# Kernel optimization log

Measured on AMD Instinct MI355X. Metric: run time of the kernel, lower is better.

Reference implementation:

```python
import jax, jax.numpy as jnp
import numpy as np

NUM_HEADS = 8
HEAD_SIZE = 64  # hidden_dim // num_heads = 512 // 8
SCALE = 1.0 / np.sqrt(HEAD_SIZE).astype(np.float32)
CAUSAL = True


def setup_inputs() -> dict:
    key = jax.random.key(0)
    k1, k2, k3 = jax.random.split(key, 3)
    b, s, d = 4, 2048, 512
    x = jax.random.normal(k1, (b, s, d), dtype=jnp.float32)
    w_qkv = jax.random.normal(k2, (d, 3 * d), dtype=jnp.float32) * 0.02
    b_qkv = jnp.zeros((3 * d,), dtype=jnp.float32)
    w_out = jax.random.normal(k3, (d, d), dtype=jnp.float32) * 0.02
    b_out = jnp.zeros((d,), dtype=jnp.float32)
    return {"x": x, "w_qkv": w_qkv, "b_qkv": b_qkv, "w_out": w_out, "b_out": b_out}


def reference(x, w_qkv, b_qkv, w_out, b_out):
    b, s, d = x.shape
    h, hd = NUM_HEADS, HEAD_SIZE
    qkv = x @ w_qkv + b_qkv                      # (b, s, 3d)
    q, k, v = jnp.split(qkv, 3, axis=-1)
    # (b, s, d) -> (b, h, s, hd)
    q = q.reshape(b, s, h, hd).transpose(0, 2, 1, 3)
    k = k.reshape(b, s, h, hd).transpose(0, 2, 1, 3)
    v = v.reshape(b, s, h, hd).transpose(0, 2, 1, 3)
    scores = jnp.einsum('bhqd,bhkd->bhqk', q, k) * SCALE  # (b, h, s, s)
    if CAUSAL:
        causal_mask = jnp.triu(jnp.ones((s, s), dtype=bool), k=1)
        scores = jnp.where(causal_mask, -jnp.inf, scores)
    attn = jax.nn.softmax(scores, axis=-1)
    out = jnp.einsum('bhqk,bhkd->bhqd', attn, v)          # (b, h, s, hd)
    out = out.transpose(0, 2, 1, 3).reshape(b, s, d)
    return out @ w_out + b_out
```

## Files before the change

kernel.cpp:

```cpp
#include <hip/hip_runtime.h>

#define BATCH 4
#define SEQ   2048
#define DM    512
#define NH    8
#define HD    64
#define PART  (BATCH*NH*SEQ*HD)
#define QSCALE 0.18033688f

typedef unsigned short u16;
typedef unsigned int   u32;
typedef __bf16 bf16x8 __attribute__((ext_vector_type(8)));
typedef float  f32x4  __attribute__((ext_vector_type(4)));

__device__ __forceinline__ u16 f2bf(float f) {
    union { float f; u32 u; } v; v.f = f;
    u32 r = v.u + 0x7fffu + ((v.u >> 16) & 1u);
    return (u16)(r >> 16);
}

__device__ __forceinline__ void glds16(const u16* g, u16* lds) {
    __builtin_amdgcn_global_load_lds(
        (const __attribute__((address_space(1))) void*)g,
        (__attribute__((address_space(3))) void*)lds, 16, 0, 0);
}

__global__ __launch_bounds__(256) void cvt_k(
    const float* __restrict__ src, u16* __restrict__ dst, int n8)
{
    for (int i = blockIdx.x * 256 + threadIdx.x; i < n8;
         i += gridDim.x * 256) {
        float4 a = *(const float4*)(src + (size_t)i * 8);
        float4 b = *(const float4*)(src + (size_t)i * 8 + 4);
        union { uint4 v; u16 s[8]; } o;
        o.s[0] = f2bf(a.x); o.s[1] = f2bf(a.y);
        o.s[2] = f2bf(a.z); o.s[3] = f2bf(a.w);
        o.s[4] = f2bf(b.x); o.s[5] = f2bf(b.y);
        o.s[6] = f2bf(b.z); o.s[7] = f2bf(b.w);
        *(uint4*)(dst + (size_t)i * 8) = o.v;
    }
}

__global__ __launch_bounds__(256) void transpose_k(
    const float* __restrict__ W0, u16* __restrict__ T0,
    const float* __restrict__ W1, u16* __restrict__ T1)
{
    const int z = blockIdx.z;
    const int N = z ? DM : 3 * DM;
    if ((int)blockIdx.x * 64 >= N) return;
    const float* W = z ? W1 : W0;
    u16* Wt = z ? T1 : T0;

    __shared__ u16 Ts[64][72];
    const int t = threadIdx.x;
    const int n0 = blockIdx.x * 64, k0 = blockIdx.y * 64;
    #pragma unroll
    for (int l = 0; l < 4; ++l) {
        int idx = l * 1024 + t * 4;
        int r = idx >> 6, c = idx & 63;
        float4 v = *(const float4*)(W + (size_t)(k0 + r) * N + n0 + c);
        Ts[c + 0][r] = f2bf(v.x);
        Ts[c + 1][r] = f2bf(v.y);
        Ts[c + 2][r] = f2bf(v.z);
        Ts[c + 3][r] = f2bf(v.w);
    }
    __syncthreads();
    #pragma unroll
    for (int l = 0; l < 2; ++l) {
        int idx = l * 256 + t;
        int row = idx >> 3, ch = idx & 7;
        *(uint4*)(Wt + (size_t)(n0 + row) * DM + k0 + ch * 8) =
            *(const uint4*)(&Ts[row][ch * 8]);
    }
}

template<int MODE>
__global__ __launch_bounds__(256) void gemm_k(
    const u16* __restrict__ A, const u16* __restrict__ Bt,
    const float* __restrict__ bias, void* __restrict__ outv,
    int M, int N, int K)
{
    __shared__ __align__(16) u16 As[128 * 32];
    __shared__ __align__(16) u16 Bs[128 * 32];

    const int tid  = threadIdx.x;
    const int bm0  = blockIdx.x * 128;
    const int bn0  = blockIdx.y * 128;
    const int wave = tid >> 6, lane = tid & 63;
    const int l16  = lane & 15, quad = lane >> 4;
    const int wr   = (wave & 1) * 64;
    const int wc   = (wave >> 1) * 64;

    const int srow = (lane >> 2);
    const int scol = (lane & 3) * 8;
    const u16* Ag = A + (size_t)(bm0 + wave * 32 + srow) * K + scol;
    const u16* Bg = Bt + (size_t)(bn0 + wave * 32 + srow) * K + scol;
    u16* AsB = &As[(wave * 32) * 32];
    u16* BsB = &Bs[(wave * 32) * 32];

    f32x4 acc[4][4];
    #pragma unroll
    for (int i = 0; i < 4; ++i)
        #pragma unroll
        for (int j = 0; j < 4; ++j)
            acc[i][j] = (f32x4){0.f, 0.f, 0.f, 0.f};

    for (int k0 = 0; k0 < K; k0 += 32) {
        glds16(Ag + k0,                  AsB);
        glds16(Ag + k0 + (size_t)16 * K, AsB + 16 * 32);
        glds16(Bg + k0,                  BsB);
        glds16(Bg + k0 + (size_t)16 * K, BsB + 16 * 32);
        __syncthreads();

        bf16x8 af[4], bfr[4];
        #pragma unroll
        for (int mi = 0; mi < 4; ++mi)
            af[mi] = *(const bf16x8*)(&As[(wr + mi * 16 + l16) * 32 + quad * 8]);
        #pragma unroll
        for (int ni = 0; ni < 4; ++ni)
            bfr[ni] = *(const bf16x8*)(&Bs[(wc + ni * 16 + l16) * 32 + quad * 8]);
        #pragma unroll
        for (int mi = 0; mi < 4; ++mi)
            #pragma unroll
            for (int ni = 0; ni < 4; ++ni)
                acc[mi][ni] = __builtin_amdgcn_mfma_f32_16x16x32_bf16(
                    af[mi], bfr[ni], acc[mi][ni], 0, 0, 0);
        __syncthreads();
    }

    #pragma unroll
    for (int mi = 0; mi < 4; ++mi) {
        #pragma unroll
        for (int ni = 0; ni < 4; ++ni) {
            int col = bn0 + wc + ni * 16 + l16;
            float bv = bias[col];
            int row0 = bm0 + wr + mi * 16 + quad * 4;
            float v[4];
            #pragma unroll
            for (int reg = 0; reg < 4; ++reg) v[reg] = acc[mi][ni][reg] + bv;

            if (MODE == 1) {
                #pragma unroll
                for (int reg = 0; reg < 4; ++reg)
                    ((float*)outv)[(size_t)(row0 + reg) * N + col] = v[reg];
            } else {
                u16* ws = (u16*)outv;
                int part = col >> 9, wi = col & 511;
                int h = wi >> 6, e = wi & 63;
                int b = row0 >> 11, s0 = row0 & 2047;
                if (part == 2) {
                    union { u16 q[4]; uint2 u; } pk;
                    #pragma unroll
                    for (int reg = 0; reg < 4; ++reg) pk.q[reg] = f2bf(v[reg]);
                    *(uint2*)(ws + (size_t)2 * PART +
                              ((size_t)(b * NH + h) * HD + e) * SEQ + s0) = pk.u;
                } else {
                    float scl = (part == 0) ? QSCALE : 1.0f;
                    #pragma unroll
                    for (int reg = 0; reg < 4; ++reg)
                        ws[(size_t)part * PART +
                           ((size_t)(b * NH + h) * SEQ + s0 + reg) * HD + e] =
                            f2bf(v[reg] * scl);
                }
            }
        }
    }
}

__global__ __launch_bounds__(256) void attn_k(
    const u16* __restrict__ Q, const u16* __restrict__ K,
    const u16* __restrict__ Vt, u16* __restrict__ O)
{
    __shared__ __align__(16) u16 KsB[2][64 * 64];
    __shared__ __align__(16) u16 VtB[2][64 * 64];
    __shared__ __align__(16) u16 Ps[128][72];

    const int bh = blockIdx.y;
    const int qb = (blockIdx.y & 16) ? (int)blockIdx.x : (15 - (int)blockIdx.x);
    const int tid = threadIdx.x, wave = tid >> 6, lane = tid & 63;
    const int l16 = lane & 15, quad = lane >> 4;
    const size_t baseK = (size_t)bh * SEQ * HD;
    const size_t baseV = (size_t)bh * HD * SEQ;
    const size_t baseQ = baseK + (size_t)qb * 128 * HD;

    #pragma unroll
    for (int r = 0; r < 4; ++r) {
        int chunk = r * 256 + tid;
        int row = chunk >> 3, c8 = (chunk & 7) << 3;
        *(uint4*)(&Ps[row][c8]) = *(const uint4*)(Q + baseQ + row * 64 + c8);
    }
    __syncthreads();

    bf16x8 qf[2][2];
    #pragma unroll
    for (int rf = 0; rf < 2; ++rf)
        #pragma unroll
        for (int d0 = 0; d0 < 2; ++d0)
            qf[rf][d0] = *(const bf16x8*)(&Ps[rf * 64 + wave * 16 + l16]
                                            [d0 * 32 + quad * 8]);

    const int sub = lane >> 3;
    const int lcx = (lane & 7) ^ sub;
    const u16* kg = K  + baseK + (size_t)((wave * 16 + sub) * 64)  + lcx * 8;
    const u16* vg = Vt + baseV + (size_t)((wave * 16 + sub) * 2048) + lcx * 8;
    u16* ksd = &KsB[0][wave * 1024];
    u16* vtd = &VtB[0][wave * 1024];

    glds16(kg,                 ksd);
    glds16(kg + 8 * 64,        ksd + 512);
    glds16(vg,                 vtd);
    glds16(vg + 8 * 2048,      vtd + 512);
    __syncthreads();

    float l_part[2][4];
    f32x4 o_acc[2][4];
    #pragma unroll
    for (int rf = 0; rf < 2; ++rf)
        #pragma unroll
        for (int i = 0; i < 4; ++i) {
            l_part[rf][i] = 0.f;
            o_acc[rf][i] = (f32x4){0.f, 0.f, 0.f, 0.f};
        }

    const int last = 2 * qb + 1;
    const int row64 = wave * 16 + quad * 4;

    for (int kt = 0; kt <= last; ++kt) {
        const int cur = kt & 1;

        if (kt < last) {
            const int nx = (cur ^ 1) * 4096;
            glds16(kg + (size_t)(kt + 1) * 4096,            ksd + nx);
            glds16(kg + (size_t)(kt + 1) * 4096 + 8 * 64,   ksd + nx + 512);
            glds16(vg + (size_t)(kt + 1) * 64,              vtd + nx);
            glds16(vg + (size_t)(kt + 1) * 64 + 8 * 2048,   vtd + nx + 512);
        }

        bf16x8 kf[2][4];
        #pragma unroll
        for (int d0 = 0; d0 < 2; ++d0)
            #pragma unroll
            for (int nt = 0; nt < 4; ++nt) {
                int pc = (d0 * 4 + quad) ^ (l16 & 7);
                kf[d0][nt] = *(const bf16x8*)
                    (&KsB[cur][(nt * 16 + l16) * 64 + pc * 8]);
            }

        #pragma unroll
        for (int rf = 0; rf < 2; ++rf) {
            if (kt == last && rf == 0) continue;
            f32x4 s[4];
            #pragma unroll
            for (int nt = 0; nt < 4; ++nt) s[nt] = (f32x4){0.f, 0.f, 0.f, 0.f};
            #pragma unroll
            for (int d0 = 0; d0 < 2; ++d0)
                #pragma unroll
                for (int nt = 0; nt < 4; ++nt)
                    s[nt] = __builtin_amdgcn_mfma_f32_16x16x32_bf16(
                        qf[rf][d0], kf[d0][nt], s[nt], 0, 0, 0);

            const bool diag = (kt == 2 * qb + rf);
            if (diag) {
                #pragma unroll
                for (int nt = 0; nt < 4; ++nt) {
                    int cl = nt * 16 + l16;
                    #pragma unroll
                    for (int reg = 0; reg < 4; ++reg) {
                        float p = (cl > row64 + reg) ? 0.f
                                : __builtin_amdgcn_exp2f(s[nt][reg]);
                        l_part[rf][reg] += p;
                        Ps[rf * 64 + row64 + reg][cl] = f2bf(p);
                    }
                }
            } else {
                #pragma unroll
                for (int nt = 0; nt < 4; ++nt) {
                    int cl = nt * 16 + l16;
                    #pragma unroll
                    for (int reg = 0; reg < 4; ++reg) {
                        float p = __builtin_amdgcn_exp2f(s[nt][reg]);
                        l_part[rf][reg] += p;
                        Ps[rf * 64 + row64 + reg][cl] = f2bf(p);
                    }
                }
            }
        }
        __syncthreads();

        bf16x8 vf[2][4];
        #pragma unroll
        for (int k0 = 0; k0 < 2; ++k0)
            #pragma unroll
            for (int dt = 0; dt < 4; ++dt) {
                int pc = (k0 * 4 + quad) ^ (l16 & 7);
                vf[k0][dt] = *(const bf16x8*)
                    (&VtB[cur][(dt * 16 + l16) * 64 + pc * 8]);
            }
        #pragma unroll
        for (int rf = 0; rf < 2; ++rf) {
            if (kt == last && rf == 0) continue;
            #pragma unroll
            for (int k0 = 0; k0 < 2; ++k0) {
                bf16x8 ap = *(const bf16x8*)
                    (&Ps[rf * 64 + wave * 16 + l16][k0 * 32 + quad * 8]);
                #pragma unroll
                for (int dt = 0; dt < 4; ++dt)
                    o_acc[rf][dt] = __builtin_amdgcn_mfma_f32_16x16x32_bf16(
                        ap, vf[k0][dt], o_acc[rf][dt], 0, 0, 0);
            }
        }
        __syncthreads();
    }

    const int b = bh >> 3, h = bh & 7;
    #pragma unroll
    for (int rf = 0; rf < 2; ++rf) {
        float l_i[4];
        #pragma unroll
        for (int reg = 0; reg < 4; ++reg) {
            float l = l_part[rf][reg];
            #pragma unroll
            for (int off = 1; off < 16; off <<= 1)
                l += __shfl_xor(l, off);
            l_i[reg] = l;
        }
        #pragma unroll
        for (int dt = 0; dt < 4; ++dt) {
            #pragma unroll
            for (int reg = 0; reg < 4; ++reg) {
                int srow = qb * 128 + rf * 64 + row64 + reg;
                float v = o_acc[rf][dt][reg] / l_i[reg];
                size_t idx = (((size_t)(b * SEQ + srow)) * NH + h) * HD
                             + dt * 16 + l16;
                O[idx] = f2bf(v);
            }
        }
    }
}

extern "C" void kernel_launch(void* const* d_in, const int* in_sizes, int n_in,
                              void* d_out, int out_size, void* d_ws, size_t ws_size,
                              hipStream_t stream) {
    const float* x     = (const float*)d_in[0];
    const float* w_qkv = (const float*)d_in[1];
    const float* b_qkv = (const float*)d_in[2];
    const float* w_out = (const float*)d_in[3];
    const float* b_out = (const float*)d_in[4];

    u16* qkv    = (u16*)d_ws;
    u16* attn   = qkv + (size_t)3 * PART;
    u16* xb     = attn + (size_t)PART;
    u16* wt_qkv = xb + (size_t)PART;
    u16* wt_out = wt_qkv + (size_t)(3 * DM) * DM;

    const int M = BATCH * SEQ;

    cvt_k<<<1024, 256, 0, stream>>>(x, xb, PART / 8);
    transpose_k<<<dim3(24, 8, 2), 256, 0, stream>>>(w_qkv, wt_qkv, w_out, wt_out);

    dim3 g1(M / 128, (3 * DM) / 128);
    gemm_k<0><<<g1, 256, 0, stream>>>(xb, wt_qkv, b_qkv, qkv, M, 3 * DM, DM);

    dim3 g2(16, BATCH * NH);
    attn_k<<<g2, 256, 0, stream>>>(qkv, qkv + PART, qkv + 2 * (size_t)PART, attn);

    dim3 g3(M / 128, DM / 128);
    gemm_k<1><<<g3, 256, 0, stream>>>(attn, wt_out, b_out, (float*)d_out, M, DM, DM);
}
```

Before: 172.2 us.

## Merge prep kernels, double-buffer GEMM LDS, drop attention sync, swap grid axes

Folds the fp32-to-bf16 conversion of x and the two weight transposes into one prep kernel launched on a 3-slice grid. The GEMM now double-buffers its A/B LDS tiles, so the next K-slice loads while MFMAs run on the current one. The attention kernel loads V fragments together with K fragments and does the P·V MFMAs right after writing P, dropping the mid-iteration barrier. This works because each wave only reads back the P rows it wrote itself. It also swaps grid axes so batch-head varies fastest, and replaces the diagonal branch with a predicated mask. The costs are extra LDS in the GEMM and more live registers in attention.

```diff
diff --git a/kernel.cpp b/kernel.cpp
--- a/kernel.cpp
+++ b/kernel.cpp
@@ -25,35 +25,35 @@
         (__attribute__((address_space(3))) void*)lds, 16, 0, 0);
 }
 
-__global__ __launch_bounds__(256) void cvt_k(
-    const float* __restrict__ src, u16* __restrict__ dst, int n8)
+__global__ __launch_bounds__(256) void prep_k(
+    const float* __restrict__ x, u16* __restrict__ xb,
+    const float* __restrict__ w_qkv, u16* __restrict__ t_qkv,
+    const float* __restrict__ w_out, u16* __restrict__ t_out)
 {
-    for (int i = blockIdx.x * 256 + threadIdx.x; i < n8;
-         i += gridDim.x * 256) {
-        float4 a = *(const float4*)(src + (size_t)i * 8);
-        float4 b = *(const float4*)(src + (size_t)i * 8 + 4);
-        union { uint4 v; u16 s[8]; } o;
-        o.s[0] = f2bf(a.x); o.s[1] = f2bf(a.y);
-        o.s[2] = f2bf(a.z); o.s[3] = f2bf(a.w);
-        o.s[4] = f2bf(b.x); o.s[5] = f2bf(b.y);
-        o.s[6] = f2bf(b.z); o.s[7] = f2bf(b.w);
-        *(uint4*)(dst + (size_t)i * 8) = o.v;
-    }
-}
-
-__global__ __launch_bounds__(256) void transpose_k(
-    const float* __restrict__ W0, u16* __restrict__ T0,
-    const float* __restrict__ W1, u16* __restrict__ T1)
-{
-    const int z = blockIdx.z;
-    const int N = z ? DM : 3 * DM;
-    if ((int)blockIdx.x * 64 >= N) return;
-    const float* W = z ? W1 : W0;
-    u16* Wt = z ? T1 : T0;
-
     __shared__ u16 Ts[64][72];
-    const int t = threadIdx.x;
-    const int n0 = blockIdx.x * 64, k0 = blockIdx.y * 64;
+    const int z = blockIdx.z, bx = blockIdx.x, t = threadIdx.x;
+
+    if (z == 0) {
+        const int n8 = PART / 8;
+        for (int i = bx * 256 + t; i < n8; i += 512 * 256) {
+            float4 a = *(const float4*)(x + (size_t)i * 8);
+            float4 b = *(const float4*)(x + (size_t)i * 8 + 4);
+            union { uint4 v; u16 s[8]; } o;
+            o.s[0] = f2bf(a.x); o.s[1] = f2bf(a.y);
+            o.s[2] = f2bf(a.z); o.s[3] = f2bf(a.w);
+            o.s[4] = f2bf(b.x); o.s[5] = f2bf(b.y);
+            o.s[6] = f2bf(b.z); o.s[7] = f2bf(b.w);
+            *(uint4*)(xb + (size_t)i * 8) = o.v;
+        }
+        return;
+    }
+    const int N = (z == 1) ? 3 * DM : DM;
+    const int ntiles = N / 64;
+    if (bx >= ntiles * 8) return;
+    const float* W = (z == 1) ? w_qkv : w_out;
+    u16* Wt = (z == 1) ? t_qkv : t_out;
+    const int n0 = (bx % ntiles) * 64, k0 = (bx / ntiles) * 64;
+
     #pragma unroll
     for (int l = 0; l < 4; ++l) {
         int idx = l * 1024 + t * 4;
@@ -80,8 +80,8 @@
     const float* __restrict__ bias, void* __restrict__ outv,
     int M, int N, int K)
 {
-    __shared__ __align__(16) u16 As[128 * 32];
-    __shared__ __align__(16) u16 Bs[128 * 32];
+    __shared__ __align__(16) u16 As[2][128 * 32];
+    __shared__ __align__(16) u16 Bs[2][128 * 32];
 
     const int tid  = threadIdx.x;
     const int bm0  = blockIdx.x * 128;
@@ -95,8 +95,7 @@
     const int scol = (lane & 3) * 8;
     const u16* Ag = A + (size_t)(bm0 + wave * 32 + srow) * K + scol;
     const u16* Bg = Bt + (size_t)(bn0 + wave * 32 + srow) * K + scol;
-    u16* AsB = &As[(wave * 32) * 32];
-    u16* BsB = &Bs[(wave * 32) * 32];
+    const int wofs = (wave * 32) * 32;
 
     f32x4 acc[4][4];
     #pragma unroll
@@ -105,20 +104,31 @@
         for (int j = 0; j < 4; ++j)
             acc[i][j] = (f32x4){0.f, 0.f, 0.f, 0.f};
 
-    for (int k0 = 0; k0 < K; k0 += 32) {
-        glds16(Ag + k0,                  AsB);
-        glds16(Ag + k0 + (size_t)16 * K, AsB + 16 * 32);
-        glds16(Bg + k0,                  BsB);
-        glds16(Bg + k0 + (size_t)16 * K, BsB + 16 * 32);
-        __syncthreads();
+    glds16(Ag,                  &As[0][wofs]);
+    glds16(Ag + (size_t)16 * K, &As[0][wofs + 16 * 32]);
+    glds16(Bg,                  &Bs[0][wofs]);
+    glds16(Bg + (size_t)16 * K, &Bs[0][wofs + 16 * 32]);
+    __syncthreads();
+
+    const int NIT = K >> 5;
+    for (int it = 0; it < NIT; ++it) {
+        const int cur = it & 1;
+        if (it + 1 < NIT) {
+            const int nx = cur ^ 1;
+            const int k0 = (it + 1) << 5;
+            glds16(Ag + k0,                  &As[nx][wofs]);
+            glds16(Ag + k0 + (size_t)16 * K, &As[nx][wofs + 16 * 32]);
+            glds16(Bg + k0,                  &Bs[nx][wofs]);
+            glds16(Bg + k0 + (size_t)16 * K, &Bs[nx][wofs + 16 * 32]);
+        }
 
         bf16x8 af[4], bfr[4];
         #pragma unroll
         for (int mi = 0; mi < 4; ++mi)
-            af[mi] = *(const bf16x8*)(&As[(wr + mi * 16 + l16) * 32 + quad * 8]);
+            af[mi] = *(const bf16x8*)(&As[cur][(wr + mi * 16 + l16) * 32 + quad * 8]);
         #pragma unroll
         for (int ni = 0; ni < 4; ++ni)
-            bfr[ni] = *(const bf16x8*)(&Bs[(wc + ni * 16 + l16) * 32 + quad * 8]);
+            bfr[ni] = *(const bf16x8*)(&Bs[cur][(wc + ni * 16 + l16) * 32 + quad * 8]);
         #pragma unroll
         for (int mi = 0; mi < 4; ++mi)
             #pragma unroll
@@ -175,8 +185,9 @@
     __shared__ __align__(16) u16 VtB[2][64 * 64];
     __shared__ __align__(16) u16 Ps[128][72];
 
-    const int bh = blockIdx.y;
-    const int qb = (blockIdx.y & 16) ? (int)blockIdx.x : (15 - (int)blockIdx.x);
+    const int bh = blockIdx.x;
+    const int yy = blockIdx.y;
+    const int qb = (yy < 8) ? (15 - yy) : (yy - 8);
     const int tid = threadIdx.x, wave = tid >> 6, lane = tid & 63;
     const int l16 = lane & 15, quad = lane >> 4;
     const size_t baseK = (size_t)bh * SEQ * HD;
@@ -201,15 +212,15 @@
 
     const int sub = lane >> 3;
     const int lcx = (lane & 7) ^ sub;
-    const u16* kg = K  + baseK + (size_t)((wave * 16 + sub) * 64)  + lcx * 8;
+    const u16* kg = K  + baseK + (size_t)((wave * 16 + sub) * 64)   + lcx * 8;
     const u16* vg = Vt + baseV + (size_t)((wave * 16 + sub) * 2048) + lcx * 8;
     u16* ksd = &KsB[0][wave * 1024];
     u16* vtd = &VtB[0][wave * 1024];
 
-    glds16(kg,                 ksd);
-    glds16(kg + 8 * 64,        ksd + 512);
-    glds16(vg,                 vtd);
-    glds16(vg + 8 * 2048,      vtd + 512);
+    glds16(kg,            ksd);
+    glds16(kg + 8 * 64,   ksd + 512);
+    glds16(vg,            vtd);
+    glds16(vg + 8 * 2048, vtd + 512);
     __syncthreads();
 
     float l_part[2][4];
@@ -230,13 +241,13 @@
 
         if (kt < last) {
             const int nx = (cur ^ 1) * 4096;
-            glds16(kg + (size_t)(kt + 1) * 4096,            ksd + nx);
-            glds16(kg + (size_t)(kt + 1) * 4096 + 8 * 64,   ksd + nx + 512);
-            glds16(vg + (size_t)(kt + 1) * 64,              vtd + nx);
-            glds16(vg + (size_t)(kt + 1) * 64 + 8 * 2048,   vtd + nx + 512);
-        }
-
-        bf16x8 kf[2][4];
+            glds16(kg + (size_t)(kt + 1) * 4096,          ksd + nx);
+            glds16(kg + (size_t)(kt + 1) * 4096 + 8 * 64, ksd + nx + 512);
+            glds16(vg + (size_t)(kt + 1) * 64,            vtd + nx);
+            glds16(vg + (size_t)(kt + 1) * 64 + 8 * 2048, vtd + nx + 512);
+        }
+
+        bf16x8 kf[2][4], vf[2][4];
         #pragma unroll
         for (int d0 = 0; d0 < 2; ++d0)
             #pragma unroll
@@ -244,6 +255,8 @@
                 int pc = (d0 * 4 + quad) ^ (l16 & 7);
                 kf[d0][nt] = *(const bf16x8*)
                     (&KsB[cur][(nt * 16 + l16) * 64 + pc * 8]);
+                vf[d0][nt] = *(const bf16x8*)
+                    (&VtB[cur][(nt * 16 + l16) * 64 + pc * 8]);
             }
 
         #pragma unroll
@@ -260,45 +273,18 @@
                         qf[rf][d0], kf[d0][nt], s[nt], 0, 0, 0);
 
             const bool diag = (kt == 2 * qb + rf);
-            if (diag) {
+            #pragma unroll
+            for (int nt = 0; nt < 4; ++nt) {
+                int cl = nt * 16 + l16;
                 #pragma unroll
-                for (int nt = 0; nt < 4; ++nt) {
-                    int cl = nt * 16 + l16;
-                    #pragma unroll
-                    for (int reg = 0; reg < 4; ++reg) {
-                        float p = (cl > row64 + reg) ? 0.f
-                                : __builtin_amdgcn_exp2f(s[nt][reg]);
-                        l_part[rf][reg] += p;
-                        Ps[rf * 64 + row64 + reg][cl] = f2bf(p);
-                    }
+                for (int reg = 0; reg < 4; ++reg) {
+                    float p = __builtin_amdgcn_exp2f(s[nt][reg]);
+                    if (diag && cl > row64 + reg) p = 0.f;
+                    l_part[rf][reg] += p;
+                    Ps[rf * 64 + row64 + reg][cl] = f2bf(p);
                 }
-            } else {
-                #pragma unroll
-                for (int nt = 0; nt < 4; ++nt) {
-                    int cl = nt * 16 + l16;
-                    #pragma unroll
-                    for (int reg = 0; reg < 4; ++reg) {
-                        float p = __builtin_amdgcn_exp2f(s[nt][reg]);
-                        l_part[rf][reg] += p;
-                        Ps[rf * 64 + row64 + reg][cl] = f2bf(p);
-                    }
-                }
-            }
-        }
-        __syncthreads();
-
-        bf16x8 vf[2][4];
-        #pragma unroll
-        for (int k0 = 0; k0 < 2; ++k0)
-            #pragma unroll
-            for (int dt = 0; dt < 4; ++dt) {
-                int pc = (k0 * 4 + quad) ^ (l16 & 7);
-                vf[k0][dt] = *(const bf16x8*)
-                    (&VtB[cur][(dt * 16 + l16) * 64 + pc * 8]);
-            }
-        #pragma unroll
-        for (int rf = 0; rf < 2; ++rf) {
-            if (kt == last && rf == 0) continue;
+            }
+
             #pragma unroll
             for (int k0 = 0; k0 < 2; ++k0) {
                 bf16x8 ap = *(const bf16x8*)
@@ -355,13 +341,13 @@
 
     const int M = BATCH * SEQ;
 
-    cvt_k<<<1024, 256, 0, stream>>>(x, xb, PART / 8);
-    transpose_k<<<dim3(24, 8, 2), 256, 0, stream>>>(w_qkv, wt_qkv, w_out, wt_out);
+    prep_k<<<dim3(512, 1, 3), 256, 0, stream>>>(x, xb, w_qkv, wt_qkv,
+                                                w_out, wt_out);
 
     dim3 g1(M / 128, (3 * DM) / 128);
     gemm_k<0><<<g1, 256, 0, stream>>>(xb, wt_qkv, b_qkv, qkv, M, 3 * DM, DM);
 
-    dim3 g2(16, BATCH * NH);
+    dim3 g2(BATCH * NH, 16);
     attn_k<<<g2, 256, 0, stream>>>(qkv, qkv + PART, qkv + 2 * (size_t)PART, attn);
 
     dim3 g3(M / 128, DM / 128);
```

Result: faster. 166.8 us (-3.1%).
